# Kernel optimization log

Hardware: AMD Instinct MI355X
Metric: run time of the kernel (lower is better)

The kernel has to match this reference:

```python
import jax, jax.numpy as jnp
import numpy as np

D = 512       # input_dim
K = 8         # output_size (number of bilinear slices)
L = 64        # hash_length
Q = 4096      # number of query vectors
C = 4096      # number of class vectors


def setup_inputs() -> dict:
    key = jax.random.key(0)
    ks = jax.random.split(key, 8)
    class_vector = jax.random.normal(ks[0], (C, D), dtype=jnp.float32)
    query_vector = jax.random.normal(ks[1], (Q, D), dtype=jnp.float32)
    # xavier_normal over (D, D, K): std = sqrt(2 / (fan_in + fan_out))
    xav = float(np.sqrt(2.0 / (D + D)))
    M = jax.random.normal(ks[2], (D, D, K), dtype=jnp.float32) * xav
    # score_layer: Linear(K, 1)
    lim_s = 1.0 / np.sqrt(K)
    score_w = jax.random.uniform(ks[3], (K,), jnp.float32, -lim_s, lim_s)
    score_b = jax.random.uniform(ks[4], (1,), jnp.float32, -lim_s, lim_s)
    # hash_layer: Linear(D, L) + Tanh
    lim_h = 1.0 / np.sqrt(D)
    hash_w = jax.random.uniform(ks[5], (L, D), jnp.float32, -lim_h, lim_h)
    hash_b = jax.random.uniform(ks[6], (L,), jnp.float32, -lim_h, lim_h)
    return {
        "class_vector": class_vector,
        "query_vector": query_vector,
        "M": M,
        "score_w": score_w,
        "score_b": score_b,
        "hash_w": hash_w,
        "hash_b": hash_b,
    }


def reference(class_vector, query_vector, M, score_w, score_b, hash_w, hash_b):
    # Looped bilinear product fused into one einsum:
    # inter_k = Q @ (C @ M[:,:,k]).T  ->  [Q, C, K]
    bi = jnp.einsum('ci,ijk,qj->qck', class_vector, M, query_vector)
    act = jax.nn.relu(bi)
    # score_layer: Linear(K, 1) then squeeze -> [Q, C]
    other = jnp.einsum('qck,k->qc', act, score_w) + score_b[0]
    relation_scores = jax.nn.softmax(other, axis=1)       # softmax over class dim
    query_features = relation_scores @ class_vector + query_vector  # [Q, D]
    hash_codes = jnp.tanh(query_features @ hash_w.T + hash_b)       # [Q, L]
    return hash_codes
```

## Files before the change

### kernel.cpp

```cpp
#include <hip/hip_runtime.h>
#include <hip/hip_bf16.h>
#include <math.h>

#define D_ 512
#define K_ 8
#define L_ 64
#define Q_ 4096
#define C_ 4096
#define N_ (C_ * K_)

typedef short short8 __attribute__((ext_vector_type(8)));
typedef float f32x4 __attribute__((ext_vector_type(4)));

static __device__ __forceinline__ void split2(float v, unsigned short& h, unsigned short& l) {
    __hip_bfloat16 hh = __float2bfloat16(v);
    float r = v - __bfloat162float(hh);
    __hip_bfloat16 ll = __float2bfloat16(r);
    h = *reinterpret_cast<unsigned short*>(&hh);
    l = *reinterpret_cast<unsigned short*>(&ll);
}

#define ASYNC_COPY16(gp, lp)                                                        \
    __builtin_amdgcn_global_load_lds((const __attribute__((address_space(1))) void*)(gp), \
                                     (__attribute__((address_space(3))) void*)(lp), \
                                     16, 0, 0)

__global__ void transpose_M_split(const float* __restrict__ M,
                                  unsigned short* __restrict__ Mh,
                                  unsigned short* __restrict__ Ml) {
    int idx = blockIdx.x * blockDim.x + threadIdx.x;
    int i = idx & (D_ - 1);
    int n2 = idx >> 9;
    int j = n2 & (D_ - 1);
    int k = n2 >> 9;
    float v = M[((size_t)i * D_ + j) * K_ + k];
    split2(v, Mh[idx], Ml[idx]);
}

__global__ void split_f32(const float* __restrict__ x,
                          unsigned short* __restrict__ hi,
                          unsigned short* __restrict__ lo) {
    int i = blockIdx.x * blockDim.x + threadIdx.x;
    split2(x[i], hi[i], lo[i]);
}

__global__ void transpose_split_classT(const float* __restrict__ x,
                                       unsigned short* __restrict__ Th,
                                       unsigned short* __restrict__ Tl) {
    int idx = blockIdx.x * blockDim.x + threadIdx.x;
    int c = idx & (C_ - 1);
    int d = idx >> 12;
    float v = x[(size_t)c * D_ + d];
    split2(v, Th[idx], Tl[idx]);
}

#define BM 128
#define BN 128
#define BNW 32
#define BKK 32

__device__ __forceinline__ void mfma_core(
    const unsigned short* __restrict__ Agh, const unsigned short* __restrict__ Agl,
    const unsigned short* __restrict__ Bgh, const unsigned short* __restrict__ Bgl,
    int lda, int ldb, int kd, int m0, int n0,
    unsigned short (*Ahb)[BM * BKK], unsigned short (*Alb)[BM * BKK],
    f32x4 acc[8][2]) {
    const int tid = threadIdx.x;
    const int lane = tid & 63;
    const int wid = tid >> 6;
    const int fr = lane & 15;
    const int fq = lane >> 4;
    const int co = (fq ^ ((fr >> 1) & 3)) * 8;

    const unsigned short* bh0 = Bgh + (size_t)(n0 + wid * BNW + fr) * ldb + fq * 8;
    const unsigned short* bl0 = Bgl + (size_t)(n0 + wid * BNW + fr) * ldb + fq * 8;

    short8 bh[2][2], bl[2][2];

#pragma unroll
    for (int h = 0; h < 2; ++h) {
        const int i2 = h * 256 + tid;
        const int r = i2 >> 2;
        const int cg = (i2 & 3) ^ ((r >> 1) & 3);
        const int ldsoff = (h * 256 + (tid & ~63)) * 8;
        const size_t go = (size_t)(m0 + r) * lda + cg * 8;
        ASYNC_COPY16(Agh + go, &Ahb[0][ldsoff]);
        ASYNC_COPY16(Agl + go, &Alb[0][ldsoff]);
    }
    bh[0][0] = *(const short8*)(bh0);
    bh[0][1] = *(const short8*)(bh0 + 16 * (size_t)ldb);
    bl[0][0] = *(const short8*)(bl0);
    bl[0][1] = *(const short8*)(bl0 + 16 * (size_t)ldb);
    __syncthreads();

    const int niter = kd / BKK;
#pragma unroll 2
    for (int it = 0; it < niter; ++it) {
        const int cur = it & 1, nxt = cur ^ 1;
        if (it + 1 < niter) {
            const int j0 = (it + 1) * BKK;
#pragma unroll
            for (int h = 0; h < 2; ++h) {
                const int i2 = h * 256 + tid;
                const int r = i2 >> 2;
                const int cg = (i2 & 3) ^ ((r >> 1) & 3);
                const int ldsoff = (h * 256 + (tid & ~63)) * 8;
                const size_t go = (size_t)(m0 + r) * lda + j0 + cg * 8;
                ASYNC_COPY16(Agh + go, &Ahb[nxt][ldsoff]);
                ASYNC_COPY16(Agl + go, &Alb[nxt][ldsoff]);
            }
            bh[nxt][0] = *(const short8*)(bh0 + j0);
            bh[nxt][1] = *(const short8*)(bh0 + 16 * (size_t)ldb + j0);
            bl[nxt][0] = *(const short8*)(bl0 + j0);
            bl[nxt][1] = *(const short8*)(bl0 + 16 * (size_t)ldb + j0);
        }
#pragma unroll
        for (int mi = 0; mi < 8; ++mi) {
            const short8 ah = *(const short8*)&Ahb[cur][(mi * 16 + fr) * BKK + co];
            const short8 al = *(const short8*)&Alb[cur][(mi * 16 + fr) * BKK + co];
#pragma unroll
            for (int ni = 0; ni < 2; ++ni) {
                acc[mi][ni] = __builtin_amdgcn_mfma_f32_16x16x32_bf16(ah, bh[cur][ni], acc[mi][ni], 0, 0, 0);
                acc[mi][ni] = __builtin_amdgcn_mfma_f32_16x16x32_bf16(ah, bl[cur][ni], acc[mi][ni], 0, 0, 0);
                acc[mi][ni] = __builtin_amdgcn_mfma_f32_16x16x32_bf16(al, bh[cur][ni], acc[mi][ni], 0, 0, 0);
            }
        }
        __syncthreads();
    }
}

#define CORE_PROLOGUE                                                            \
    __shared__ __attribute__((aligned(16))) unsigned short Ahb[2][BM * BKK];     \
    __shared__ __attribute__((aligned(16))) unsigned short Alb[2][BM * BKK];     \
    const int tid = threadIdx.x;                                                 \
    const int lane = tid & 63;                                                   \
    const int wid = tid >> 6;                                                    \
    const int fr = lane & 15;                                                    \
    const int fq = lane >> 4;                                                    \
    f32x4 acc[8][2] = {};                                                        \
    (void)tid;

__launch_bounds__(256, 3)
__global__ void gemm_P_mfma(const unsigned short* __restrict__ Chh,
                            const unsigned short* __restrict__ Cll,
                            const unsigned short* __restrict__ Mh,
                            const unsigned short* __restrict__ Ml,
                            unsigned short* __restrict__ Ph,
                            unsigned short* __restrict__ Pl) {
    CORE_PROLOGUE
    const int n0 = blockIdx.x * BN;
    const int c0 = blockIdx.y * BM;
    mfma_core(Chh, Cll, Mh, Ml, D_, D_, D_, c0, n0, Ahb, Alb, acc);
#pragma unroll
    for (int mi = 0; mi < 8; ++mi)
#pragma unroll
        for (int ni = 0; ni < 2; ++ni)
#pragma unroll
            for (int r = 0; r < 4; ++r) {
                int c = c0 + mi * 16 + fq * 4 + r;
                int n2 = n0 + wid * BNW + ni * 16 + fr;
                size_t o = (size_t)c * (K_ * D_) + n2;
                split2(acc[mi][ni][r], Ph[o], Pl[o]);
            }
}

__launch_bounds__(256, 3)
__global__ void bilinear_mfma(const unsigned short* __restrict__ Qh,
                              const unsigned short* __restrict__ Ql,
                              const unsigned short* __restrict__ Ph,
                              const unsigned short* __restrict__ Pl,
                              const float* __restrict__ sw,
                              const float* __restrict__ sb,
                              float* __restrict__ other) {
    CORE_PROLOGUE
    const int n0 = blockIdx.x * BN;
    const int q0 = blockIdx.y * BM;
    mfma_core(Qh, Ql, Ph, Pl, D_, D_, D_, q0, n0, Ahb, Alb, acc);
    const float wk = sw[lane & 7];
    const float bias = sb[0];
#pragma unroll
    for (int mi = 0; mi < 8; ++mi)
#pragma unroll
        for (int ni = 0; ni < 2; ++ni)
#pragma unroll
            for (int r = 0; r < 4; ++r) {
                float v = wk * fmaxf(acc[mi][ni][r], 0.f);
                v += __shfl_xor(v, 1);
                v += __shfl_xor(v, 2);
                v += __shfl_xor(v, 4);
                if ((lane & 7) == 0) {
                    int q = q0 + mi * 16 + fq * 4 + r;
                    int c = (n0 + wid * BNW + ni * 16 + fr) >> 3;
                    other[(size_t)q * C_ + c] = v + bias;
                }
            }
}

__launch_bounds__(256, 3)
__global__ void gemm_qf_mfma(const unsigned short* __restrict__ Sh,
                             const unsigned short* __restrict__ Sl,
                             const unsigned short* __restrict__ Th,
                             const unsigned short* __restrict__ Tl,
                             float* __restrict__ qfp0,
                             float* __restrict__ qfp1) {
    CORE_PROLOGUE
    const int n0 = blockIdx.x * BN;
    const int q0 = blockIdx.y * BM;
    const int zoff = blockIdx.z * (C_ / 2);
    float* qfp = blockIdx.z ? qfp1 : qfp0;
    mfma_core(Sh + zoff, Sl + zoff, Th + zoff, Tl + zoff,
              C_, C_, C_ / 2, q0, n0, Ahb, Alb, acc);
#pragma unroll
    for (int mi = 0; mi < 8; ++mi)
#pragma unroll
        for (int ni = 0; ni < 2; ++ni)
#pragma unroll
            for (int r = 0; r < 4; ++r) {
                int q = q0 + mi * 16 + fq * 4 + r;
                int d = n0 + wid * BNW + ni * 16 + fr;
                qfp[(size_t)q * D_ + d] = acc[mi][ni][r];
            }
}

__launch_bounds__(256)
__global__ void softmax_split(const float* __restrict__ other,
                              unsigned short* __restrict__ Sh,
                              unsigned short* __restrict__ Sl) {
    const int q = blockIdx.x;
    const float* row = other + (size_t)q * C_;
    const int tid = threadIdx.x;
    __shared__ float red[4];
    float v[16];
    float m = -1e30f;
#pragma unroll
    for (int it = 0; it < 16; ++it) {
        v[it] = row[tid + it * 256];
        m = fmaxf(m, v[it]);
    }
#pragma unroll
    for (int off = 32; off; off >>= 1) m = fmaxf(m, __shfl_down(m, off));
    if ((tid & 63) == 0) red[tid >> 6] = m;
    __syncthreads();
    m = fmaxf(fmaxf(red[0], red[1]), fmaxf(red[2], red[3]));
    __syncthreads();
    float s = 0.f;
#pragma unroll
    for (int it = 0; it < 16; ++it) {
        v[it] = __expf(v[it] - m);
        s += v[it];
    }
#pragma unroll
    for (int off = 32; off; off >>= 1) s += __shfl_down(s, off);
    if ((tid & 63) == 0) red[tid >> 6] = s;
    __syncthreads();
    const float inv = 1.f / (red[0] + red[1] + red[2] + red[3]);
#pragma unroll
    for (int it = 0; it < 16; ++it) {
        size_t o = (size_t)q * C_ + tid + it * 256;
        split2(v[it] * inv, Sh[o], Sl[o]);
    }
}

__launch_bounds__(256)
__global__ void hash_kernel(const float* __restrict__ qfp0,
                            const float* __restrict__ qfp1,
                            const float* __restrict__ Qv,
                            const float* __restrict__ hw,
                            const float* __restrict__ hb,
                            float* __restrict__ out) {
    __shared__ float sqf[4 * D_];
    const int q0 = blockIdx.x * 4;
    const int tid = threadIdx.x;
    {
        const float4* s0 = (const float4*)&qfp0[(size_t)q0 * D_];
        const float4* s1 = (const float4*)&qfp1[(size_t)q0 * D_];
        const float4* s2 = (const float4*)&Qv[(size_t)q0 * D_];
        float4* dst = (float4*)sqf;
#pragma unroll
        for (int it = 0; it < 2; ++it) {
            int i = tid + it * 256;
            float4 a = s0[i], b = s1[i], c = s2[i];
            float4 o = {a.x + b.x + c.x, a.y + b.y + c.y,
                        a.z + b.z + c.z, a.w + b.w + c.w};
            dst[i] = o;
        }
    }
    __syncthreads();
    const int l = tid % L_;
    const int qi = tid / L_;
    float s = hb[l];
    const float* wrow = &hw[(size_t)l * D_];
    const float* xrow = &sqf[qi * D_];
#pragma unroll 4
    for (int d = 0; d < D_; d += 4) {
        float4 w4 = *(const float4*)&wrow[d];
        float4 x4 = *(const float4*)&xrow[d];
        s += x4.x * w4.x + x4.y * w4.y + x4.z * w4.z + x4.w * w4.w;
    }
    out[(size_t)(q0 + qi) * L_ + l] = tanhf(s);
}

extern "C" void kernel_launch(void* const* d_in, const int* in_sizes, int n_in,
                              void* d_out, int out_size, void* d_ws, size_t ws_size,
                              hipStream_t stream) {
    const float* class_v = (const float*)d_in[0];
    const float* query_v = (const float*)d_in[1];
    const float* M       = (const float*)d_in[2];
    const float* score_w = (const float*)d_in[3];
    const float* score_b = (const float*)d_in[4];
    const float* hash_w  = (const float*)d_in[5];
    const float* hash_b  = (const float*)d_in[6];
    float* out = (float*)d_out;

    char* base = (char*)d_ws;
    unsigned short* Ph = (unsigned short*)base;
    unsigned short* Pl = (unsigned short*)(base + (size_t)33554432);
    char* oreg          = base + (size_t)67108864;
    float* other        = (float*)oreg;
    unsigned short* Mh  = (unsigned short*)oreg;
    unsigned short* Ml  = (unsigned short*)(oreg + (size_t)4194304);
    unsigned short* Chh = (unsigned short*)(oreg + (size_t)8388608);
    unsigned short* Cll = (unsigned short*)(oreg + (size_t)12582912);
    float* qfp0         = (float*)oreg;
    float* qfp1         = (float*)(oreg + (size_t)8388608);
    char* scratch = base + (size_t)134217728;
    unsigned short* Qh = (unsigned short*)scratch;
    unsigned short* Ql = (unsigned short*)(scratch + (size_t)4194304);
    unsigned short* Th = (unsigned short*)scratch;
    unsigned short* Tl = (unsigned short*)(scratch + (size_t)4194304);
    unsigned short* Sh = Ph;
    unsigned short* Sl = Pl;

    transpose_M_split<<<(K_ * D_ * D_) / 256, 256, 0, stream>>>(M, Mh, Ml);
    split_f32<<<(C_ * D_) / 256, 256, 0, stream>>>(class_v, Chh, Cll);
    split_f32<<<(Q_ * D_) / 256, 256, 0, stream>>>(query_v, Qh, Ql);
    gemm_P_mfma<<<dim3((K_ * D_) / BN, C_ / BM), 256, 0, stream>>>(Chh, Cll, Mh, Ml, Ph, Pl);
    bilinear_mfma<<<dim3(N_ / BN, Q_ / BM), 256, 0, stream>>>(Qh, Ql, Ph, Pl,
                                                              score_w, score_b, other);
    softmax_split<<<Q_, 256, 0, stream>>>(other, Sh, Sl);
    transpose_split_classT<<<(C_ * D_) / 256, 256, 0, stream>>>(class_v, Th, Tl);
    gemm_qf_mfma<<<dim3(D_ / BN, Q_ / BM, 2), 256, 0, stream>>>(Sh, Sl, Th, Tl, qfp0, qfp1);
    hash_kernel<<<Q_ / 4, 256, 0, stream>>>(qfp0, qfp1, query_v, hash_w, hash_b, out);
}
```

Baseline: 779.0 us.

## Reorder bilinear grid, raise occupancy bounds, and split query-feature GEMM four ways

The bilinear GEMM grid is transposed so that consecutive blocks walk along the query dimension while sharing one P column tile. This is meant to improve L2 and MALL reuse of the large P operand, with the small split query operand staying cache-resident. The launch-bounds minimum blocks per SM rises from 3 to 4 on the three MFMA GEMMs, which may force register spills. The softmax-times-class GEMM goes from 2-way to 4-way split-K to fill more CUs, at the cost of extra partial buffers the hash kernel must read and sum.

```diff
diff --git a/kernel.cpp b/kernel.cpp
--- a/kernel.cpp
+++ b/kernel.cpp
@@ -140,7 +140,7 @@
     f32x4 acc[8][2] = {};                                                        \
     (void)tid;
 
-__launch_bounds__(256, 3)
+__launch_bounds__(256, 4)
 __global__ void gemm_P_mfma(const unsigned short* __restrict__ Chh,
                             const unsigned short* __restrict__ Cll,
                             const unsigned short* __restrict__ Mh,
@@ -164,7 +164,7 @@
             }
 }
 
-__launch_bounds__(256, 3)
+__launch_bounds__(256, 4)
 __global__ void bilinear_mfma(const unsigned short* __restrict__ Qh,
                               const unsigned short* __restrict__ Ql,
                               const unsigned short* __restrict__ Ph,
@@ -173,8 +173,8 @@
                               const float* __restrict__ sb,
                               float* __restrict__ other) {
     CORE_PROLOGUE
-    const int n0 = blockIdx.x * BN;
-    const int q0 = blockIdx.y * BM;
+    const int q0 = blockIdx.x * BM;
+    const int n0 = blockIdx.y * BN;
     mfma_core(Qh, Ql, Ph, Pl, D_, D_, D_, q0, n0, Ahb, Alb, acc);
     const float wk = sw[lane & 7];
     const float bias = sb[0];
@@ -196,20 +196,19 @@
             }
 }
 
-__launch_bounds__(256, 3)
+__launch_bounds__(256, 4)
 __global__ void gemm_qf_mfma(const unsigned short* __restrict__ Sh,
                              const unsigned short* __restrict__ Sl,
                              const unsigned short* __restrict__ Th,
                              const unsigned short* __restrict__ Tl,
-                             float* __restrict__ qfp0,
-                             float* __restrict__ qfp1) {
+                             float* __restrict__ qfp_base) {
     CORE_PROLOGUE
     const int n0 = blockIdx.x * BN;
     const int q0 = blockIdx.y * BM;
-    const int zoff = blockIdx.z * (C_ / 2);
-    float* qfp = blockIdx.z ? qfp1 : qfp0;
+    const int zoff = blockIdx.z * (C_ / 4);
+    float* qfp = qfp_base + (size_t)blockIdx.z * Q_ * D_;
     mfma_core(Sh + zoff, Sl + zoff, Th + zoff, Tl + zoff,
-              C_, C_, C_ / 2, q0, n0, Ahb, Alb, acc);
+              C_, C_, C_ / 4, q0, n0, Ahb, Alb, acc);
 #pragma unroll
     for (int mi = 0; mi < 8; ++mi)
 #pragma unroll
@@ -262,8 +261,7 @@
 }
 
 __launch_bounds__(256)
-__global__ void hash_kernel(const float* __restrict__ qfp0,
-                            const float* __restrict__ qfp1,
+__global__ void hash_kernel(const float* __restrict__ qfp_base,
                             const float* __restrict__ Qv,
                             const float* __restrict__ hw,
                             const float* __restrict__ hb,
@@ -272,16 +270,18 @@
     const int q0 = blockIdx.x * 4;
     const int tid = threadIdx.x;
     {
-        const float4* s0 = (const float4*)&qfp0[(size_t)q0 * D_];
-        const float4* s1 = (const float4*)&qfp1[(size_t)q0 * D_];
-        const float4* s2 = (const float4*)&Qv[(size_t)q0 * D_];
+        const float4* s0 = (const float4*)&qfp_base[(size_t)q0 * D_];
+        const float4* s1 = (const float4*)&qfp_base[(size_t)Q_ * D_ + q0 * D_];
+        const float4* s2 = (const float4*)&qfp_base[(size_t)2 * Q_ * D_ + q0 * D_];
+        const float4* s3 = (const float4*)&qfp_base[(size_t)3 * Q_ * D_ + q0 * D_];
+        const float4* s4 = (const float4*)&Qv[(size_t)q0 * D_];
         float4* dst = (float4*)sqf;
 #pragma unroll
         for (int it = 0; it < 2; ++it) {
             int i = tid + it * 256;
-            float4 a = s0[i], b = s1[i], c = s2[i];
-            float4 o = {a.x + b.x + c.x, a.y + b.y + c.y,
-                        a.z + b.z + c.z, a.w + b.w + c.w};
+            float4 a = s0[i], b = s1[i], c = s2[i], d = s3[i], e = s4[i];
+            float4 o = {a.x + b.x + c.x + d.x + e.x, a.y + b.y + c.y + d.y + e.y,
+                        a.z + b.z + c.z + d.z + e.z, a.w + b.w + c.w + d.w + e.w};
             dst[i] = o;
         }
     }
@@ -321,8 +321,7 @@
     unsigned short* Ml  = (unsigned short*)(oreg + (size_t)4194304);
     unsigned short* Chh = (unsigned short*)(oreg + (size_t)8388608);
     unsigned short* Cll = (unsigned short*)(oreg + (size_t)12582912);
-    float* qfp0         = (float*)oreg;
-    float* qfp1         = (float*)(oreg + (size_t)8388608);
+    float* qfp          = (float*)oreg;
     char* scratch = base + (size_t)134217728;
     unsigned short* Qh = (unsigned short*)scratch;
     unsigned short* Ql = (unsigned short*)(scratch + (size_t)4194304);
@@ -335,10 +334,10 @@
     split_f32<<<(C_ * D_) / 256, 256, 0, stream>>>(class_v, Chh, Cll);
     split_f32<<<(Q_ * D_) / 256, 256, 0, stream>>>(query_v, Qh, Ql);
     gemm_P_mfma<<<dim3((K_ * D_) / BN, C_ / BM), 256, 0, stream>>>(Chh, Cll, Mh, Ml, Ph, Pl);
-    bilinear_mfma<<<dim3(N_ / BN, Q_ / BM), 256, 0, stream>>>(Qh, Ql, Ph, Pl,
+    bilinear_mfma<<<dim3(Q_ / BM, N_ / BN), 256, 0, stream>>>(Qh, Ql, Ph, Pl,
                                                               score_w, score_b, other);
     softmax_split<<<Q_, 256, 0, stream>>>(other, Sh, Sl);
     transpose_split_classT<<<(C_ * D_) / 256, 256, 0, stream>>>(class_v, Th, Tl);
-    gemm_qf_mfma<<<dim3(D_ / BN, Q_ / BM, 2), 256, 0, stream>>>(Sh, Sl, Th, Tl, qfp0, qfp1);
-    hash_kernel<<<Q_ / 4, 256, 0, stream>>>(qfp0, qfp1, query_v, hash_w, hash_b, out);
-}
+    gemm_qf_mfma<<<dim3(D_ / BN, Q_ / BM, 4), 256, 0, stream>>>(Sh, Sl, Th, Tl, qfp);
+    hash_kernel<<<Q_ / 4, 256, 0, stream>>>(qfp, query_v, hash_w, hash_b, out);
+}
```

Measured after the change: 758.9 us. 2.6% less time.
